# Performance work log

Measured on AMD Instinct MI355X. Metric: run time of the kernel, lower is better.

## Reference

```python
import jax, jax.numpy as jnp
import numpy as np

B, D, A, R = 256, 1024, 1024, 8  # batch, feat_dim, ada_dim, rank
I = A  # inter_dim defaults to ada_dim
LN_EPS = 1e-5


def setup_inputs() -> dict:
    key = jax.random.key(0)
    ks = jax.random.split(key, 5)
    return {
        "x": jax.random.normal(ks[0], (B, D), jnp.float32),
        "ada_emb": jax.random.normal(ks[1], (B, A), jnp.float32),
        "base_layer": jax.random.normal(ks[2], (D, D), jnp.float32) * 0.02,
        "ln_gamma": jnp.ones((A,), jnp.float32),
        "ln_beta": jnp.zeros((A,), jnp.float32),
        "W1": jax.random.normal(ks[3], (A, I), jnp.float32) * 0.02,
        "b1": jnp.zeros((I,), jnp.float32),
        "W2": jax.random.normal(ks[4], (I, D * R * 2), jnp.float32) * 0.02,
        "b2": jnp.zeros((D * R * 2,), jnp.float32),
    }


def reference(x, ada_emb, base_layer, ln_gamma, ln_beta, W1, b1, W2, b2):
    Bc, Dc = x.shape
    # norm_cond: LayerNorm over ada_dim
    mu = jnp.mean(ada_emb, axis=-1, keepdims=True)
    var = jnp.var(ada_emb, axis=-1, keepdims=True)
    cond = (ada_emb - mu) * jax.lax.rsqrt(var + LN_EPS) * ln_gamma + ln_beta
    # gen_weight: Linear -> GELU (exact, erf) -> Linear
    h = jax.nn.gelu(cond @ W1 + b1, approximate=False)
    w = h @ W2 + b2                      # [B, 2*D*R]
    x_a, x_b = jnp.split(w, 2, axis=-1)
    x_a = x_a.reshape(Bc, Dc, R)         # [B, D, R]
    x_b = x_b.reshape(Bc, Dc, R)         # [B, D, R]
    # per-sample low-rank weight added to the shared base layer
    layer = base_layer[None, :, :] + jnp.einsum('bdr,bkr->bdk', x_a, x_b)  # [B, D, D]
    out = jnp.einsum('bc,bco->bo', x, layer)
    return x + out  # residual=True
```

## Files before the change

### kernel.cpp

```cpp
#include <hip/hip_runtime.h>
#include <math.h>

#define BB 256
#define DD 1024
#define AA 1024
#define RR 8
#define II 1024
#define NOUT (2*DD*RR)
#define LN_EPS 1e-5f

typedef __attribute__((ext_vector_type(8))) short bf16x8;
typedef __attribute__((ext_vector_type(8))) unsigned short ushort8;
typedef __attribute__((ext_vector_type(4))) float f32x4;

typedef const __attribute__((address_space(1))) unsigned int gu32_t;
typedef __attribute__((address_space(3))) unsigned int lu32_t;

__device__ __forceinline__ void glds16(void* lds, const void* g) {
    __builtin_amdgcn_global_load_lds((gu32_t*)g, (lu32_t*)lds, 16, 0, 0);
}

__device__ __forceinline__ f32x4 mfma16(bf16x8 a, bf16x8 b, f32x4 c) {
    return __builtin_amdgcn_mfma_f32_16x16x32_bf16(a, b, c, 0, 0, 0);
}

__device__ __forceinline__ unsigned short f2bf(float x) {
    unsigned int u = __float_as_uint(x);
    unsigned int r = (u + 0x7fffu + ((u >> 16) & 1u)) >> 16;
    return (unsigned short)r;
}
__device__ __forceinline__ float bf2f(unsigned short b) {
    return __uint_as_float(((unsigned int)b) << 16);
}
__device__ __forceinline__ void split2(float x, unsigned short& hi, unsigned short& lo) {
    hi = f2bf(x);
    lo = f2bf(x - bf2f(hi));
}

__device__ __forceinline__ float gelu_exact(float v) {
    return 0.5f * v * (1.0f + erff(v * 0.70710678118654752f));
}

__device__ __forceinline__ void region_top_wait() {
    asm volatile("s_waitcnt vmcnt(0) lgkmcnt(0)" ::: "memory");
    __builtin_amdgcn_sched_barrier(0);
    __builtin_amdgcn_s_barrier();
    __builtin_amdgcn_sched_barrier(0);
}
__device__ __forceinline__ void region_end_wait() {
    asm volatile("s_waitcnt lgkmcnt(0)" ::: "memory");
    __builtin_amdgcn_sched_barrier(0);
}

__global__ __launch_bounds__(256) void ln_split_kernel(const float* __restrict__ ada,
                                                       const float* __restrict__ xp,
                                                       const float* __restrict__ gamma,
                                                       const float* __restrict__ beta,
                                                       char* __restrict__ c_t,
                                                       char* __restrict__ x_t) {
    const int b = blockIdx.x;
    const int tid = threadIdx.x;
    const float4 v = ((const float4*)(ada + (size_t)b * AA))[tid];

    float s  = v.x + v.y + v.z + v.w;
    float ss = v.x * v.x + v.y * v.y + v.z * v.z + v.w * v.w;
    #pragma unroll
    for (int off = 32; off; off >>= 1) {
        s  += __shfl_down(s, off);
        ss += __shfl_down(ss, off);
    }
    __shared__ float red[2][4];
    const int wid = tid >> 6, lane = tid & 63;
    if (lane == 0) { red[0][wid] = s; red[1][wid] = ss; }
    __syncthreads();
    __shared__ float stats[2];
    if (tid == 0) {
        float S  = red[0][0] + red[0][1] + red[0][2] + red[0][3];
        float SS = red[1][0] + red[1][1] + red[1][2] + red[1][3];
        float mu  = S * (1.0f / AA);
        float var = SS * (1.0f / AA) - mu * mu;
        stats[0] = mu;
        stats[1] = rsqrtf(var + LN_EPS);
    }
    __syncthreads();
    const float mu = stats[0], inv = stats[1];
    const float4 g  = ((const float4*)gamma)[tid];
    const float4 be = ((const float4*)beta)[tid];

    const int k0 = tid * 4;
    const int mbh = (b >> 4) & 1;
    const size_t img = ((size_t)(b >> 5) * 16 + (k0 >> 6)) * 8192;
    const int inoff = ((k0 >> 3) & 7) * 256 + (b & 15) * 16 + (k0 & 7) * 2;

    float o[4];
    o[0] = (v.x - mu) * inv * g.x + be.x;
    o[1] = (v.y - mu) * inv * g.y + be.y;
    o[2] = (v.z - mu) * inv * g.z + be.z;
    o[3] = (v.w - mu) * inv * g.w + be.w;
    ushort4 H, L;
    split2(o[0], H.x, L.x); split2(o[1], H.y, L.y);
    split2(o[2], H.z, L.z); split2(o[3], H.w, L.w);
    *(ushort4*)(c_t + img + (0 * 2 + mbh) * 2048 + inoff) = H;
    *(ushort4*)(c_t + img + (1 * 2 + mbh) * 2048 + inoff) = L;

    const float4 xv = ((const float4*)(xp + (size_t)b * DD))[tid];
    split2(xv.x, H.x, L.x); split2(xv.y, H.y, L.y);
    split2(xv.z, H.z, L.z); split2(xv.w, H.w, L.w);
    *(ushort4*)(x_t + img + (0 * 2 + mbh) * 2048 + inoff) = H;
    *(ushort4*)(x_t + img + (1 * 2 + mbh) * 2048 + inoff) = L;
}

__global__ __launch_bounds__(256) void gemm_small(const char* __restrict__ x_t,
                                                  const char* __restrict__ c_t,
                                                  const float* __restrict__ base,
                                                  const float* __restrict__ W1,
                                                  const float* __restrict__ b1,
                                                  float* __restrict__ outy,
                                                  char* __restrict__ h_t) {
    __shared__ __align__(16) char As[2][8192];
    __shared__ __align__(16) char Bs[2][16384];

    const int z = blockIdx.z;
    const char* __restrict__ At = z ? c_t : x_t;
    const float* __restrict__ Bsrc = z ? W1 : base;

    const int tid = threadIdx.x;
    const int bn = blockIdx.x * 64;
    const int bm = blockIdx.y * 32;
    const int wid = tid >> 6, l = tid & 63;
    const int kg = l >> 4, lr16 = (l & 15) * 16;

    f32x4 acc[2];
    acc[0] = (f32x4)0.0f; acc[1] = (f32x4)0.0f;

    const int sn = tid & 63;
    const int sk0 = (tid >> 6) * 16;
    const int s_nb = sn >> 4, s_l16 = (sn & 15) * 16;

    float v[16];

    #define SB_LOAD(KT)                                                          \
        _Pragma("unroll")                                                        \
        for (int j = 0; j < 16; j++)                                             \
            v[j] = Bsrc[(size_t)((KT) * 64 + sk0 + j) * 1024 + bn + sn];

    #define SB_WRITE(BUF)                                                        \
        _Pragma("unroll")                                                        \
        for (int h2 = 0; h2 < 2; h2++) {                                         \
            const int kidx = (sk0 >> 3) + h2;                                    \
            ushort8 H, L;                                                        \
            _Pragma("unroll")                                                    \
            for (int j = 0; j < 8; j++) { unsigned short hh, ll;                 \
                split2(v[h2 * 8 + j], hh, ll); H[j] = hh; L[j] = ll; }           \
            *(ushort8*)(Bs[BUF] + ((0*4 + s_nb)*8 + kidx)*256 + s_l16) = H;      \
            *(ushort8*)(Bs[BUF] + ((1*4 + s_nb)*8 + kidx)*256 + s_l16) = L;      \
        }

    #define SA_GLDS(BUF, KT)                                                     \
        {                                                                        \
            const char* ib = At + ((size_t)(bm >> 5) * 16 + (KT)) * 8192;        \
            _Pragma("unroll")                                                    \
            for (int c = 0; c < 2; c++) {                                        \
                const int ch = wid * 2 + c;                                      \
                glds16(As[BUF] + ch * 1024, ib + ch * 1024 + l * 16);            \
            }                                                                    \
        }

    #define S_COMPUTE(BUF)                                                       \
        _Pragma("unroll")                                                        \
        for (int s2 = 0; s2 < 2; s2++) {                                         \
            bf16x8 a[2][2], bbf[2];                                              \
            _Pragma("unroll")                                                    \
            for (int pl = 0; pl < 2; pl++) {                                     \
                _Pragma("unroll")                                                \
                for (int mi = 0; mi < 2; mi++)                                   \
                    a[pl][mi] = *(const bf16x8*)(As[BUF] +                       \
                        ((pl*2 + mi)*8 + s2*4 + kg)*256 + lr16);                 \
                bbf[pl] = *(const bf16x8*)(Bs[BUF] +                             \
                        ((pl*4 + wid)*8 + s2*4 + kg)*256 + lr16);                \
            }                                                                    \
            _Pragma("unroll")                                                    \
            for (int mi = 0; mi < 2; mi++) {                                     \
                acc[mi] = mfma16(a[0][mi], bbf[0], acc[mi]);                     \
                acc[mi] = mfma16(a[0][mi], bbf[1], acc[mi]);                     \
                acc[mi] = mfma16(a[1][mi], bbf[0], acc[mi]);                     \
            }                                                                    \
        }

    SB_LOAD(0);
    SA_GLDS(0, 0);
    SB_WRITE(0);

    for (int t = 0; t < 16; ++t) {
        const int cur = t & 1;
        region_top_wait();
        if (t < 15) {
            SB_LOAD(t + 1);
            SA_GLDS(cur ^ 1, t + 1);
        }
        S_COMPUTE(cur);
        if (t < 15) {
            SB_WRITE(cur ^ 1);
        }
        region_end_wait();
    }

    #pragma unroll
    for (int mi = 0; mi < 2; mi++) {
        const int row0 = bm + mi * 16 + kg * 4;
        const int col  = bn + wid * 16 + (l & 15);
        #pragma unroll
        for (int j = 0; j < 4; j++) {
            float val = acc[mi][j];
            const int row = row0 + j;
            if (z == 0) {
                outy[(size_t)row * 1024 + col] = val;
            } else {
                float g = gelu_exact(val + b1[col]);
                unsigned short hi, lo;
                split2(g, hi, lo);
                char* ib = h_t + ((size_t)(row >> 7) * 32 + (col >> 5)) * 16384;
                const int inoff = (((row >> 4) & 7) * 4 + ((col >> 3) & 3)) * 256
                                + (row & 15) * 16 + (col & 7) * 2;
                *(unsigned short*)(ib + 0 * 8192 + inoff) = hi;
                *(unsigned short*)(ib + 1 * 8192 + inoff) = lo;
            }
        }
    }
    #undef SB_LOAD
    #undef SB_WRITE
    #undef SA_GLDS
    #undef S_COMPUTE
}

__global__ __launch_bounds__(512) void gemm_big(const char* __restrict__ h_t,
                                                const float* __restrict__ Bm,
                                                const float* __restrict__ bias,
                                                float* __restrict__ Cm) {
    __shared__ __align__(16) char As[2][16384];
    __shared__ __align__(16) char Bs[2][16384];

    const int tid = threadIdx.x;
    const int bn = blockIdx.x * 128;
    const int bm = blockIdx.y * 128;
    const int wid = tid >> 6, l = tid & 63;
    const int wm = wid >> 2, wn = wid & 3;
    const int kg = l >> 4, lr16 = (l & 15) * 16;

    f32x4 acc[4][2];
    #pragma unroll
    for (int i = 0; i < 4; i++) { acc[i][0] = (f32x4)0.0f; acc[i][1] = (f32x4)0.0f; }

    const int sn = tid & 127;
    const int skg = tid >> 7;
    const int s_nb = sn >> 4, s_l16 = (sn & 15) * 16;

    float v[8];

    #define GB_LOAD(KT)                                                          \
        _Pragma("unroll")                                                        \
        for (int j = 0; j < 8; j++)                                              \
            v[j] = Bm[(size_t)((KT) * 32 + skg * 8 + j) * NOUT + bn + sn];

    #define GB_WRITE(BUF)                                                        \
        {                                                                        \
            ushort8 H, L;                                                        \
            _Pragma("unroll")                                                    \
            for (int j = 0; j < 8; j++) { unsigned short hh, ll;                 \
                split2(v[j], hh, ll); H[j] = hh; L[j] = ll; }                    \
            *(ushort8*)(Bs[BUF] + ((0*8 + s_nb)*4 + skg)*256 + s_l16) = H;       \
            *(ushort8*)(Bs[BUF] + ((1*8 + s_nb)*4 + skg)*256 + s_l16) = L;       \
        }

    #define GA_GLDS(BUF, KT)                                                     \
        {                                                                        \
            const char* ib = h_t + ((size_t)(bm >> 7) * 32 + (KT)) * 16384;      \
            _Pragma("unroll")                                                    \
            for (int c = 0; c < 2; c++) {                                        \
                const int ch = wid * 2 + c;                                      \
                glds16(As[BUF] + ch * 1024, ib + ch * 1024 + l * 16);            \
            }                                                                    \
        }

    #define G_COMPUTE(BUF)                                                       \
        {                                                                        \
            bf16x8 a[2][4], bbf[2][2];                                           \
            _Pragma("unroll")                                                    \
            for (int pl = 0; pl < 2; pl++) {                                     \
                _Pragma("unroll")                                                \
                for (int mi = 0; mi < 4; mi++)                                   \
                    a[pl][mi] = *(const bf16x8*)(As[BUF] +                       \
                        ((pl*8 + wm*4 + mi)*4 + kg)*256 + lr16);                 \
                _Pragma("unroll")                                                \
                for (int ni = 0; ni < 2; ni++)                                   \
                    bbf[pl][ni] = *(const bf16x8*)(Bs[BUF] +                     \
                        ((pl*8 + wn*2 + ni)*4 + kg)*256 + lr16);                 \
            }                                                                    \
            __builtin_amdgcn_s_setprio(1);                                       \
            _Pragma("unroll")                                                    \
            for (int mi = 0; mi < 4; mi++) {                                     \
                _Pragma("unroll")                                                \
                for (int ni = 0; ni < 2; ni++) {                                 \
                    acc[mi][ni] = mfma16(a[0][mi], bbf[0][ni], acc[mi][ni]);     \
                    acc[mi][ni] = mfma16(a[0][mi], bbf[1][ni], acc[mi][ni]);     \
                    acc[mi][ni] = mfma16(a[1][mi], bbf[0][ni], acc[mi][ni]);     \
                }                                                                \
            }                                                                    \
            __builtin_amdgcn_s_setprio(0);                                       \
        }

    GB_LOAD(0);
    GA_GLDS(0, 0);
    GB_WRITE(0);

    for (int t = 0; t < 32; ++t) {
        const int cur = t & 1;
        region_top_wait();
        if (t < 31) {
            GB_LOAD(t + 1);
            GA_GLDS(cur ^ 1, t + 1);
        }
        G_COMPUTE(cur);
        if (t < 31) {
            GB_WRITE(cur ^ 1);
        }
        region_end_wait();
    }

    #pragma unroll
    for (int mi = 0; mi < 4; mi++) {
        #pragma unroll
        for (int ni = 0; ni < 2; ni++) {
            const int row0 = bm + wm * 64 + mi * 16 + kg * 4;
            const int col  = bn + wn * 32 + ni * 16 + (l & 15);
            const float bv = bias[col];
            #pragma unroll
            for (int j = 0; j < 4; j++)
                Cm[(size_t)(row0 + j) * NOUT + col] = acc[mi][ni][j] + bv;
        }
    }
    #undef GB_LOAD
    #undef GB_WRITE
    #undef GA_GLDS
    #undef G_COMPUTE
}

__global__ __launch_bounds__(256) void tail_kernel(const float* __restrict__ x,
                                                   const float* __restrict__ w,
                                                   float* __restrict__ out) {
    const int b = blockIdx.x;
    const int tid = threadIdx.x;
    const float* wa = w + (size_t)b * NOUT;
    const float4 xv = ((const float4*)(x + (size_t)b * DD))[tid];
    const float xs[4] = {xv.x, xv.y, xv.z, xv.w};

    float acc[RR] = {};
    #pragma unroll
    for (int i = 0; i < 4; i++) {
        const int c = tid * 4 + i;
        const float4 w0 = *(const float4*)&wa[c * RR];
        const float4 w1 = *(const float4*)&wa[c * RR + 4];
        acc[0] = fmaf(xs[i], w0.x, acc[0]);
        acc[1] = fmaf(xs[i], w0.y, acc[1]);
        acc[2] = fmaf(xs[i], w0.z, acc[2]);
        acc[3] = fmaf(xs[i], w0.w, acc[3]);
        acc[4] = fmaf(xs[i], w1.x, acc[4]);
        acc[5] = fmaf(xs[i], w1.y, acc[5]);
        acc[6] = fmaf(xs[i], w1.z, acc[6]);
        acc[7] = fmaf(xs[i], w1.w, acc[7]);
    }
    __shared__ float red[4][RR];
    __shared__ float trs[RR];
    const int wid = tid >> 6, lane = tid & 63;
    #pragma unroll
    for (int r = 0; r < RR; r++) {
        float vv = acc[r];
        #pragma unroll
        for (int off = 32; off; off >>= 1) vv += __shfl_down(vv, off);
        if (lane == 0) red[wid][r] = vv;
    }
    __syncthreads();
    if (tid < RR) trs[tid] = red[0][tid] + red[1][tid] + red[2][tid] + red[3][tid];
    __syncthreads();

    float tr[RR];
    #pragma unroll
    for (int r = 0; r < RR; r++) tr[r] = trs[r];

    const float* wb = wa + DD * RR;
    const int o0 = tid * 4;
    const float4 yv = *(const float4*)&out[(size_t)b * DD + o0];

    float vals[4];
    #pragma unroll
    for (int i = 0; i < 4; i++) {
        const float4 w0 = *(const float4*)&wb[(o0 + i) * RR];
        const float4 w1 = *(const float4*)&wb[(o0 + i) * RR + 4];
        vals[i] = tr[0] * w0.x + tr[1] * w0.y + tr[2] * w0.z + tr[3] * w0.w
                + tr[4] * w1.x + tr[5] * w1.y + tr[6] * w1.z + tr[7] * w1.w;
    }
    float4 o;
    o.x = xv.x + yv.x + vals[0];
    o.y = xv.y + yv.y + vals[1];
    o.z = xv.z + yv.z + vals[2];
    o.w = xv.w + yv.w + vals[3];
    *(float4*)&out[(size_t)b * DD + o0] = o;
}

extern "C" void kernel_launch(void* const* d_in, const int* in_sizes, int n_in,
                              void* d_out, int out_size, void* d_ws, size_t ws_size,
                              hipStream_t stream) {
    const float* x     = (const float*)d_in[0];
    const float* ada   = (const float*)d_in[1];
    const float* base  = (const float*)d_in[2];
    const float* gamma = (const float*)d_in[3];
    const float* beta  = (const float*)d_in[4];
    const float* W1    = (const float*)d_in[5];
    const float* b1    = (const float*)d_in[6];
    const float* W2    = (const float*)d_in[7];
    const float* b2    = (const float*)d_in[8];
    float* out = (float*)d_out;

    char* wsb = (char*)d_ws;
    float* w  = (float*)(wsb);
    char* h_t = wsb + 16777216;
    char* x_t = wsb + 17825792;
    char* c_t = wsb + 18874368;

    ln_split_kernel<<<BB, 256, 0, stream>>>(ada, x, gamma, beta, c_t, x_t);

    gemm_small<<<dim3(1024 / 64, BB / 32, 2), 256, 0, stream>>>(
        x_t, c_t, base, W1, b1, out, h_t);

    gemm_big<<<dim3(NOUT / 128, BB / 128), 512, 0, stream>>>(h_t, W2, b2, w);

    tail_kernel<<<BB, 256, 0, stream>>>(x, w, out);
}
```

Measured before the change: 178.0 us.

## Retile gemm_big to 128x64 blocks with swizzle and relax pipeline waits

gemm_big shrinks its output tile from 128x128 with 512 threads to 128x64 with 256 threads. It launches 512 blocks on a 1D grid, remapped with a swizzle so that blocks sharing W2 columns run close together. In both GEMM kernels the full vmcnt(0) drain at the top of each iteration becomes a partial vmcnt wait, so that iteration's new prefetch loads can stay in flight while compute runs. gemm_small also raises wave priority around its MFMA block. The aim is better CU occupancy and overlap of loads with compute on the W2 stream. The cost is that the h tile is fetched twice as often and the hand-counted vmcnt values are fragile.

```diff
diff --git a/kernel.cpp b/kernel.cpp
--- a/kernel.cpp
+++ b/kernel.cpp
@@ -41,14 +41,9 @@
     return 0.5f * v * (1.0f + erff(v * 0.70710678118654752f));
 }
 
-__device__ __forceinline__ void region_top_wait() {
-    asm volatile("s_waitcnt vmcnt(0) lgkmcnt(0)" ::: "memory");
+__device__ __forceinline__ void bar() {
     __builtin_amdgcn_sched_barrier(0);
     __builtin_amdgcn_s_barrier();
-    __builtin_amdgcn_sched_barrier(0);
-}
-__device__ __forceinline__ void region_end_wait() {
-    asm volatile("s_waitcnt lgkmcnt(0)" ::: "memory");
     __builtin_amdgcn_sched_barrier(0);
 }
 
@@ -179,30 +174,38 @@
                 bbf[pl] = *(const bf16x8*)(Bs[BUF] +                             \
                         ((pl*4 + wid)*8 + s2*4 + kg)*256 + lr16);                \
             }                                                                    \
+            __builtin_amdgcn_s_setprio(1);                                       \
             _Pragma("unroll")                                                    \
             for (int mi = 0; mi < 2; mi++) {                                     \
                 acc[mi] = mfma16(a[0][mi], bbf[0], acc[mi]);                     \
                 acc[mi] = mfma16(a[0][mi], bbf[1], acc[mi]);                     \
                 acc[mi] = mfma16(a[1][mi], bbf[0], acc[mi]);                     \
             }                                                                    \
+            __builtin_amdgcn_s_setprio(0);                                       \
         }
 
     SB_LOAD(0);
     SA_GLDS(0, 0);
     SB_WRITE(0);
+    asm volatile("s_waitcnt lgkmcnt(0)" ::: "memory");
+    bar();
 
     for (int t = 0; t < 16; ++t) {
         const int cur = t & 1;
-        region_top_wait();
         if (t < 15) {
             SB_LOAD(t + 1);
             SA_GLDS(cur ^ 1, t + 1);
-        }
+            asm volatile("s_waitcnt vmcnt(18)" ::: "memory");
+        } else {
+            asm volatile("s_waitcnt vmcnt(0)" ::: "memory");
+        }
+        bar();
         S_COMPUTE(cur);
         if (t < 15) {
             SB_WRITE(cur ^ 1);
         }
-        region_end_wait();
+        asm volatile("s_waitcnt lgkmcnt(0)" ::: "memory");
+        bar();
     }
 
     #pragma unroll
@@ -233,26 +236,29 @@
     #undef S_COMPUTE
 }
 
-__global__ __launch_bounds__(512) void gemm_big(const char* __restrict__ h_t,
+__global__ __launch_bounds__(256) void gemm_big(const char* __restrict__ h_t,
                                                 const float* __restrict__ Bm,
                                                 const float* __restrict__ bias,
                                                 float* __restrict__ Cm) {
     __shared__ __align__(16) char As[2][16384];
-    __shared__ __align__(16) char Bs[2][16384];
+    __shared__ __align__(16) char Bs[2][8192];
+
+    const int hw = blockIdx.x;
+    const int swz = ((hw & 7) << 6) + (hw >> 3);
+    const int bn = (swz >> 1) * 64;
+    const int bm = (swz & 1) * 128;
 
     const int tid = threadIdx.x;
-    const int bn = blockIdx.x * 128;
-    const int bm = blockIdx.y * 128;
     const int wid = tid >> 6, l = tid & 63;
-    const int wm = wid >> 2, wn = wid & 3;
+    const int wm = wid >> 1, wn = wid & 1;
     const int kg = l >> 4, lr16 = (l & 15) * 16;
 
     f32x4 acc[4][2];
     #pragma unroll
     for (int i = 0; i < 4; i++) { acc[i][0] = (f32x4)0.0f; acc[i][1] = (f32x4)0.0f; }
 
-    const int sn = tid & 127;
-    const int skg = tid >> 7;
+    const int sn = tid & 63;
+    const int skc = tid >> 6;
     const int s_nb = sn >> 4, s_l16 = (sn & 15) * 16;
 
     float v[8];
@@ -260,7 +266,7 @@
     #define GB_LOAD(KT)                                                          \
         _Pragma("unroll")                                                        \
         for (int j = 0; j < 8; j++)                                              \
-            v[j] = Bm[(size_t)((KT) * 32 + skg * 8 + j) * NOUT + bn + sn];
+            v[j] = Bm[(size_t)((KT) * 32 + skc * 8 + j) * NOUT + bn + sn];
 
     #define GB_WRITE(BUF)                                                        \
         {                                                                        \
@@ -268,16 +274,16 @@
             _Pragma("unroll")                                                    \
             for (int j = 0; j < 8; j++) { unsigned short hh, ll;                 \
                 split2(v[j], hh, ll); H[j] = hh; L[j] = ll; }                    \
-            *(ushort8*)(Bs[BUF] + ((0*8 + s_nb)*4 + skg)*256 + s_l16) = H;       \
-            *(ushort8*)(Bs[BUF] + ((1*8 + s_nb)*4 + skg)*256 + s_l16) = L;       \
+            *(ushort8*)(Bs[BUF] + ((0*4 + s_nb)*4 + skc)*256 + s_l16) = H;       \
+            *(ushort8*)(Bs[BUF] + ((1*4 + s_nb)*4 + skc)*256 + s_l16) = L;       \
         }
 
     #define GA_GLDS(BUF, KT)                                                     \
         {                                                                        \
             const char* ib = h_t + ((size_t)(bm >> 7) * 32 + (KT)) * 16384;      \
             _Pragma("unroll")                                                    \
-            for (int c = 0; c < 2; c++) {                                        \
-                const int ch = wid * 2 + c;                                      \
+            for (int c = 0; c < 4; c++) {                                        \
+                const int ch = wid * 4 + c;                                      \
                 glds16(As[BUF] + ch * 1024, ib + ch * 1024 + l * 16);            \
             }                                                                    \
         }
@@ -294,7 +300,7 @@
                 _Pragma("unroll")                                                \
                 for (int ni = 0; ni < 2; ni++)                                   \
                     bbf[pl][ni] = *(const bf16x8*)(Bs[BUF] +                     \
-                        ((pl*8 + wn*2 + ni)*4 + kg)*256 + lr16);                 \
+                        ((pl*4 + wn*2 + ni)*4 + kg)*256 + lr16);                 \
             }                                                                    \
             __builtin_amdgcn_s_setprio(1);                                       \
             _Pragma("unroll")                                                    \
@@ -312,19 +318,25 @@
     GB_LOAD(0);
     GA_GLDS(0, 0);
     GB_WRITE(0);
+    asm volatile("s_waitcnt lgkmcnt(0)" ::: "memory");
+    bar();
 
     for (int t = 0; t < 32; ++t) {
         const int cur = t & 1;
-        region_top_wait();
         if (t < 31) {
             GB_LOAD(t + 1);
             GA_GLDS(cur ^ 1, t + 1);
-        }
+            asm volatile("s_waitcnt vmcnt(12)" ::: "memory");
+        } else {
+            asm volatile("s_waitcnt vmcnt(0)" ::: "memory");
+        }
+        bar();
         G_COMPUTE(cur);
         if (t < 31) {
             GB_WRITE(cur ^ 1);
         }
-        region_end_wait();
+        asm volatile("s_waitcnt lgkmcnt(0)" ::: "memory");
+        bar();
     }
 
     #pragma unroll
@@ -432,7 +444,7 @@
     gemm_small<<<dim3(1024 / 64, BB / 32, 2), 256, 0, stream>>>(
         x_t, c_t, base, W1, b1, out, h_t);
 
-    gemm_big<<<dim3(NOUT / 128, BB / 128), 512, 0, stream>>>(h_t, W2, b2, w);
+    gemm_big<<<512, 256, 0, stream>>>(h_t, W2, b2, w);
 
     tail_kernel<<<BB, 256, 0, stream>>>(x, w, out);
 }
```

Result: no change. 178.6 us (+0.3%).
